# Kernel optimization log

Hardware: AMD Instinct MI355X
Metric: run time of the kernel (lower is better)

Reference implementation:

```python
import jax, jax.numpy as jnp
import numpy as np

N_NODES = 50000
N_EDGES = 800000
D = 128


def setup_inputs() -> dict:
    key = jax.random.key(0)
    ks = jax.random.split(key, 5)
    x = jax.random.normal(ks[0], (N_NODES, D), dtype=jnp.float32)
    edge_index = jax.random.randint(ks[1], (2, N_EDGES), 0, N_NODES, dtype=jnp.int64)
    # GCNConv linear weight + bias, and the two DGCN parameters
    Wc = jax.random.normal(ks[2], (D, D), dtype=jnp.float32) / np.sqrt(D)
    bc = jnp.zeros((D,), dtype=jnp.float32)
    W0 = jax.random.normal(ks[3], (D, D), dtype=jnp.float32)
    Wt = jax.random.normal(ks[4], (D, D), dtype=jnp.float32)
    return {"x": x, "edge_index": edge_index, "Wc": Wc, "bc": bc, "W0": W0, "Wt": Wt}


def gcn_conv(x, edge_index, Wc, bc):
    # PyG GCNConv: add self-loops, symmetric normalization D^-1/2 (A+I) D^-1/2,
    # applied to x @ Wc, plus bias.
    n = x.shape[0]
    loops = jnp.arange(n, dtype=edge_index.dtype)
    src = jnp.concatenate([edge_index[0], loops])  # [E+N]
    dst = jnp.concatenate([edge_index[1], loops])
    ones = jnp.ones(src.shape[0], dtype=x.dtype)
    deg = jax.ops.segment_sum(ones, dst, num_segments=n)  # in-degree incl. self-loop
    dinv = jnp.where(deg > 0, jax.lax.rsqrt(deg), 0.0)
    norm = dinv[src] * dinv[dst]  # [E+N]
    xw = x @ Wc  # [N, D]
    msgs = xw[src] * norm[:, None]  # gather + scale  [E+N, D]
    agg = jax.ops.segment_sum(msgs, dst, num_segments=n)  # scatter-add  [N, D]
    return agg + bc


def reference(x, edge_index, Wc, bc, W0, Wt):
    h_neigh = gcn_conv(x, edge_index, Wc, bc)
    h_self = x @ W0
    h_change = (h_neigh - x) @ Wt
    return h_neigh + h_self + h_change
```

## Files before the change

### kernel.cpp

```cpp
#include <hip/hip_runtime.h>

#define N_NODES 50000
#define N_EDGES 800000
#define D 128
#define NB 196
#define P1_BLOCKS 128
#define EPB ((N_EDGES + P1_BLOCKS - 1) / P1_BLOCKS)
#define CAP 64

typedef __attribute__((ext_vector_type(8))) short short8;
typedef __attribute__((ext_vector_type(4))) float f32x4;

__device__ __forceinline__ unsigned short f2bf(float f) {
    unsigned int u = __builtin_bit_cast(unsigned int, f);
    u += 0x7FFFu + ((u >> 16) & 1u);
    return (unsigned short)(u >> 16);
}
__device__ __forceinline__ float bf2f(unsigned short h) {
    unsigned int u = ((unsigned int)h) << 16;
    return __builtin_bit_cast(float, u);
}

__global__ __launch_bounds__(256) void k_bcnt(const int* __restrict__ dst,
                                              int* __restrict__ bcnt) {
    __shared__ int h[NB];
    const int t = threadIdx.x;
    for (int i = t; i < NB; i += 256) h[i] = 0;
    __syncthreads();
    const long e0 = (long)blockIdx.x * EPB;
    const long e1 = (e0 + EPB < N_EDGES) ? e0 + EPB : N_EDGES;
    for (long e = e0 + t; e < e1; e += 256) atomicAdd(&h[dst[e] >> 8], 1);
    __syncthreads();
    for (int i = t; i < NB; i += 256)
        if (h[i]) atomicAdd(&bcnt[i], h[i]);
}

__global__ __launch_bounds__(256) void k_bscan2(const int* __restrict__ bcnt,
                                                int* __restrict__ bucket_base,
                                                int* __restrict__ gcur) {
    __shared__ int s[256];
    const int t = threadIdx.x;
    const int v = (t < NB) ? bcnt[t] : 0;
    s[t] = v;
    __syncthreads();
    for (int off = 1; off < 256; off <<= 1) {
        int u = (t >= off) ? s[t - off] : 0;
        __syncthreads();
        s[t] += u;
        __syncthreads();
    }
    if (t < NB) {
        const int base = s[t] - v;
        bucket_base[t] = base;
        gcur[t] = base;
    }
}

__global__ __launch_bounds__(256) void k_part1(const int* __restrict__ src,
                                               const int* __restrict__ dst,
                                               int* __restrict__ gcur,
                                               unsigned int* __restrict__ pbuf) {
    __shared__ unsigned int stage[NB][CAP + 1];
    __shared__ int scnt[NB];
    const int t = threadIdx.x;
    for (int i = t; i < NB; i += 256) scnt[i] = 0;
    __syncthreads();

    const long e0 = (long)blockIdx.x * EPB;
    const long e1 = (e0 + EPB < N_EDGES) ? e0 + EPB : N_EDGES;
    for (long e = e0 + t; e < e1; e += 256) {
        const int s = src[e];
        const int d = dst[e];
        const int b = d >> 8;
        const unsigned int p = ((unsigned int)(d & 255) << 16) | (unsigned int)s;
        const int slot = atomicAdd(&scnt[b], 1);
        if (slot < CAP) {
            stage[b][slot] = p;
        } else {
            const int pos = atomicAdd(&gcur[b], 1);
            pbuf[pos] = p;
        }
    }
    __syncthreads();
    if (t < NB) {
        const int n = (scnt[t] < CAP) ? scnt[t] : CAP;
        if (n > 0) {
            const int pos = atomicAdd(&gcur[t], n);
            for (int i = 0; i < n; ++i) pbuf[pos + i] = stage[t][i];
        }
    }
}

__global__ __launch_bounds__(256) void k_part2(const unsigned int* __restrict__ pbuf,
                                               const int* __restrict__ bucket_base,
                                               const int* __restrict__ bcnt,
                                               int* __restrict__ row_start,
                                               int* __restrict__ cnt,
                                               float* __restrict__ dinv,
                                               int* __restrict__ esrc) {
    __shared__ int lcnt[256];
    __shared__ int lcur[256];
    __shared__ int stmp[256];
    const int b = blockIdx.x;
    const int t = threadIdx.x;
    const int base = bucket_base[b];
    const int n = bcnt[b];

    lcnt[t] = 0;
    __syncthreads();
    for (int i = t; i < n; i += 256) atomicAdd(&lcnt[pbuf[base + i] >> 16], 1);
    __syncthreads();

    const int c = lcnt[t];
    stmp[t] = c;
    __syncthreads();
    for (int off = 1; off < 256; off <<= 1) {
        int u = (t >= off) ? stmp[t - off] : 0;
        __syncthreads();
        stmp[t] += u;
        __syncthreads();
    }
    const int ls = base + stmp[t] - c;
    lcur[t] = ls;
    const int node = b * 256 + t;
    if (node < N_NODES) {
        row_start[node] = ls;
        cnt[node] = c;
        dinv[node] = rsqrtf((float)c + 1.0f);
    }
    __syncthreads();

    for (int i = t; i < n; i += 256) {
        const unsigned int p = pbuf[base + i];
        const int pos = atomicAdd(&lcur[p >> 16], 1);
        esrc[pos] = (int)(p & 0xFFFFu);
    }
}

__global__ __launch_bounds__(256) void k_wpack(const float* __restrict__ Wc,
                                               const float* __restrict__ W0,
                                               const float* __restrict__ Wt,
                                               const float* __restrict__ bc,
                                               unsigned short* __restrict__ Wp,
                                               float* __restrict__ bv) {
    __shared__ float sWt[D * D];
    const int t = threadIdx.x;
    for (int i = t * 4; i < D * D; i += 256 * 4)
        *(float4*)(sWt + i) = *(const float4*)(Wt + i);
    __syncthreads();

    if (blockIdx.x == 16) {
        if (t < D) {
            float acc = bc[t];
#pragma unroll 16
            for (int k = 0; k < D; ++k) acc += bc[k] * sWt[k * D + t];
            bv[t] = acc;
        }
        return;
    }
    const int id = blockIdx.x * 256 + t;
    const int lane = id & 63;
    const int tile = (id >> 6) & 7;
    const int step = id >> 9;
    const int n = tile * 16 + (lane & 15);
    const int kbase = step * 32 + (lane >> 4) * 8;
    unsigned short v[8];
#pragma unroll
    for (int j = 0; j < 8; ++j) {
        const int k = kbase + j;
        float f;
        if (k < D) {
            f = Wc[k * D + n];
#pragma unroll 16
            for (int m = 0; m < D; ++m) f += Wc[k * D + m] * sWt[m * D + n];
        } else {
            f = W0[(k - D) * D + n] - sWt[(k - D) * D + n];
        }
        v[j] = f2bf(f);
    }
    *(uint4*)(Wp + (long)id * 8) = *(uint4*)v;
}

__global__ __launch_bounds__(256) void k_xcast(const float* __restrict__ x,
                                               const float* __restrict__ dinv,
                                               unsigned short* __restrict__ xd,
                                               unsigned short* __restrict__ gx) {
    const int gid = blockIdx.x * 256 + threadIdx.x;
    const int node = gid >> 4;
    const int c = gid & 15;
    const float di = dinv[node];
    const float4 a = ((const float4*)x)[(long)node * 32 + c * 2];
    const float4 b = ((const float4*)x)[(long)node * 32 + c * 2 + 1];
    const float f[8] = {a.x, a.y, a.z, a.w, b.x, b.y, b.z, b.w};
    unsigned short vd[8], vb[8];
#pragma unroll
    for (int j = 0; j < 8; ++j) {
        vd[j] = f2bf(di * f[j]);
        vb[j] = f2bf(f[j]);
    }
    *(uint4*)(xd + (long)node * 128 + c * 8) = *(uint4*)vd;
    *(uint4*)(gx + (long)node * 256 + 128 + c * 8) = *(uint4*)vb;
}

__global__ __launch_bounds__(256) void k_gather(const unsigned short* __restrict__ xd,
                                                const int* __restrict__ row_start,
                                                const int* __restrict__ cnt,
                                                const int* __restrict__ esrc,
                                                const float* __restrict__ dinv,
                                                unsigned short* __restrict__ gx) {
    const int node = blockIdx.x * 4 + (threadIdx.x >> 6);
    const int lane = threadIdx.x & 63;
    const int c = lane & 15;
    const int s = lane >> 4;
    const int begin = row_start[node];
    const int end = begin + cnt[node];

    float acc[8] = {};
    int i = begin + s;
    for (; i + 4 < end; i += 8) {
        const int a0 = esrc[i];
        const int a1 = esrc[i + 4];
        const short8 v0 = *(const short8*)(xd + (long)a0 * 128 + c * 8);
        const short8 v1 = *(const short8*)(xd + (long)a1 * 128 + c * 8);
#pragma unroll
        for (int j = 0; j < 8; ++j)
            acc[j] += bf2f((unsigned short)v0[j]) + bf2f((unsigned short)v1[j]);
    }
    if (i < end) {
        const int a0 = esrc[i];
        const short8 v0 = *(const short8*)(xd + (long)a0 * 128 + c * 8);
#pragma unroll
        for (int j = 0; j < 8; ++j) acc[j] += bf2f((unsigned short)v0[j]);
    }

#pragma unroll
    for (int j = 0; j < 8; ++j) {
        acc[j] += __shfl_xor(acc[j], 16);
        acc[j] += __shfl_xor(acc[j], 32);
    }

    if (s == 0) {
        const float di = dinv[node];
        const short8 xs = *(const short8*)(xd + (long)node * 128 + c * 8);
        unsigned short o[8];
#pragma unroll
        for (int j = 0; j < 8; ++j)
            o[j] = f2bf(di * (acc[j] + bf2f((unsigned short)xs[j])));
        *(uint4*)(gx + (long)node * 256 + c * 8) = *(uint4*)o;
    }
}

__global__ __launch_bounds__(256) void k_mm(const unsigned short* __restrict__ gx,
                                            const unsigned short* __restrict__ Wp,
                                            const float* __restrict__ bv,
                                            float* __restrict__ out) {
    const int tid = threadIdx.x;
    const int wave = tid >> 6;
    const int lane = tid & 63;
    const int quad = lane >> 4;
    const int lr = lane & 15;
    const int row0 = blockIdx.x * 64 + wave * 16;

    int ar = row0 + lr;
    if (ar >= N_NODES) ar = N_NODES - 1;
    const unsigned short* aptr = gx + (long)ar * 256 + quad * 8;

    f32x4 acc[8] = {};

#pragma unroll
    for (int s = 0; s < 8; ++s) {
        const short8 a = *(const short8*)(aptr + s * 32);
#pragma unroll
        for (int t = 0; t < 8; ++t) {
            const short8 b = *(const short8*)(Wp + ((long)(s * 8 + t) * 64 + lane) * 8);
            acc[t] = __builtin_amdgcn_mfma_f32_16x16x32_bf16(a, b, acc[t], 0, 0, 0);
        }
    }

#pragma unroll
    for (int t = 0; t < 8; ++t) {
        const int col = t * 16 + lr;
        const float bvv = bv[col];
#pragma unroll
        for (int r = 0; r < 4; ++r) {
            const int row = row0 + quad * 4 + r;
            if (row < N_NODES) out[(long)row * D + col] = acc[t][r] + bvv;
        }
    }
}

extern "C" void kernel_launch(void* const* d_in, const int* in_sizes, int n_in,
                              void* d_out, int out_size, void* d_ws, size_t ws_size,
                              hipStream_t stream) {
    const float* x  = (const float*)d_in[0];
    const int*   ei = (const int*)d_in[1];
    const float* Wc = (const float*)d_in[2];
    const float* bc = (const float*)d_in[3];
    const float* W0 = (const float*)d_in[4];
    const float* Wt = (const float*)d_in[5];
    float* out = (float*)d_out;

    const int* src = ei;
    const int* dst = ei + N_EDGES;

    unsigned short* gx = (unsigned short*)d_ws;
    unsigned short* xd = gx + (size_t)N_NODES * 256;
    int*   cnt        = (int*)(xd + (size_t)N_NODES * 128);
    int*   row_start  = cnt + N_NODES;
    float* dinv       = (float*)(row_start + N_NODES);
    int*   esrc       = (int*)(dinv + N_NODES);
    unsigned int* pbuf = (unsigned int*)(esrc + N_EDGES);
    float* bv         = (float*)(pbuf + N_EDGES);
    unsigned short* Wp = (unsigned short*)(bv + D);
    int*   bcnt       = (int*)(Wp + 256 * D);
    int*   bucket_base = bcnt + NB;
    int*   gcur       = bucket_base + NB;

    hipMemsetAsync(bcnt, 0, NB * sizeof(int), stream);

    k_bcnt<<<P1_BLOCKS, 256, 0, stream>>>(dst, bcnt);
    k_bscan2<<<1, 256, 0, stream>>>(bcnt, bucket_base, gcur);
    k_part1<<<P1_BLOCKS, 256, 0, stream>>>(src, dst, gcur, pbuf);
    k_part2<<<NB, 256, 0, stream>>>(pbuf, bucket_base, bcnt, row_start, cnt, dinv, esrc);

    k_wpack<<<17, 256, 0, stream>>>(Wc, W0, Wt, bc, Wp, bv);

    k_xcast<<<(N_NODES * 16) / 256, 256, 0, stream>>>(x, dinv, xd, gx);

    k_gather<<<N_NODES / 4, 256, 0, stream>>>(xd, row_start, cnt, esrc, dinv, gx);

    k_mm<<<(N_NODES + 63) / 64, 256, 0, stream>>>(gx, Wp, bv, out);
}
```

Baseline: 197.8 us.

## Fuse neighbor gather into MFMA matmul, drop bucket-count pass, merge weight-pack and cast

```diff
diff --git a/kernel.cpp b/kernel.cpp
--- a/kernel.cpp
+++ b/kernel.cpp
@@ -4,9 +4,11 @@
 #define N_EDGES 800000
 #define D 128
 #define NB 196
+#define CAPB 8192
 #define P1_BLOCKS 128
 #define EPB ((N_EDGES + P1_BLOCKS - 1) / P1_BLOCKS)
 #define CAP 64
+#define GROWS 136
 
 typedef __attribute__((ext_vector_type(8))) short short8;
 typedef __attribute__((ext_vector_type(4))) float f32x4;
@@ -21,39 +23,9 @@
     return __builtin_bit_cast(float, u);
 }
 
-__global__ __launch_bounds__(256) void k_bcnt(const int* __restrict__ dst,
-                                              int* __restrict__ bcnt) {
-    __shared__ int h[NB];
+__global__ void k_init(int* __restrict__ gcur) {
     const int t = threadIdx.x;
-    for (int i = t; i < NB; i += 256) h[i] = 0;
-    __syncthreads();
-    const long e0 = (long)blockIdx.x * EPB;
-    const long e1 = (e0 + EPB < N_EDGES) ? e0 + EPB : N_EDGES;
-    for (long e = e0 + t; e < e1; e += 256) atomicAdd(&h[dst[e] >> 8], 1);
-    __syncthreads();
-    for (int i = t; i < NB; i += 256)
-        if (h[i]) atomicAdd(&bcnt[i], h[i]);
-}
-
-__global__ __launch_bounds__(256) void k_bscan2(const int* __restrict__ bcnt,
-                                                int* __restrict__ bucket_base,
-                                                int* __restrict__ gcur) {
-    __shared__ int s[256];
-    const int t = threadIdx.x;
-    const int v = (t < NB) ? bcnt[t] : 0;
-    s[t] = v;
-    __syncthreads();
-    for (int off = 1; off < 256; off <<= 1) {
-        int u = (t >= off) ? s[t - off] : 0;
-        __syncthreads();
-        s[t] += u;
-        __syncthreads();
-    }
-    if (t < NB) {
-        const int base = s[t] - v;
-        bucket_base[t] = base;
-        gcur[t] = base;
-    }
+    if (t < NB) gcur[t] = t * CAPB;
 }
 
 __global__ __launch_bounds__(256) void k_part1(const int* __restrict__ src,
@@ -92,8 +64,7 @@
 }
 
 __global__ __launch_bounds__(256) void k_part2(const unsigned int* __restrict__ pbuf,
-                                               const int* __restrict__ bucket_base,
-                                               const int* __restrict__ bcnt,
+                                               const int* __restrict__ gcur,
                                                int* __restrict__ row_start,
                                                int* __restrict__ cnt,
                                                float* __restrict__ dinv,
@@ -103,8 +74,8 @@
     __shared__ int stmp[256];
     const int b = blockIdx.x;
     const int t = threadIdx.x;
-    const int base = bucket_base[b];
-    const int n = bcnt[b];
+    const int base = b * CAPB;
+    const int n = gcur[b] - base;
 
     lcnt[t] = 0;
     __syncthreads();
@@ -137,55 +108,58 @@
     }
 }
 
-__global__ __launch_bounds__(256) void k_wpack(const float* __restrict__ Wc,
-                                               const float* __restrict__ W0,
-                                               const float* __restrict__ Wt,
-                                               const float* __restrict__ bc,
-                                               unsigned short* __restrict__ Wp,
-                                               float* __restrict__ bv) {
+__global__ __launch_bounds__(256) void k_wx(const float* __restrict__ Wc,
+                                            const float* __restrict__ W0,
+                                            const float* __restrict__ Wt,
+                                            const float* __restrict__ bc,
+                                            const float* __restrict__ x,
+                                            const float* __restrict__ dinv,
+                                            unsigned short* __restrict__ Wp,
+                                            float* __restrict__ bv,
+                                            unsigned short* __restrict__ xd,
+                                            unsigned short* __restrict__ xb) {
     __shared__ float sWt[D * D];
     const int t = threadIdx.x;
-    for (int i = t * 4; i < D * D; i += 256 * 4)
-        *(float4*)(sWt + i) = *(const float4*)(Wt + i);
-    __syncthreads();
-
-    if (blockIdx.x == 16) {
-        if (t < D) {
-            float acc = bc[t];
+
+    if (blockIdx.x < 17) {
+        for (int i = t * 4; i < D * D; i += 256 * 4)
+            *(float4*)(sWt + i) = *(const float4*)(Wt + i);
+        __syncthreads();
+
+        if (blockIdx.x == 16) {
+            if (t < D) {
+                float acc = bc[t];
 #pragma unroll 16
-            for (int k = 0; k < D; ++k) acc += bc[k] * sWt[k * D + t];
-            bv[t] = acc;
-        }
+                for (int k = 0; k < D; ++k) acc += bc[k] * sWt[k * D + t];
+                bv[t] = acc;
+            }
+            return;
+        }
+        const int id = blockIdx.x * 256 + t;
+        const int lane = id & 63;
+        const int tile = (id >> 6) & 7;
+        const int step = id >> 9;
+        const int n = tile * 16 + (lane & 15);
+        const int kbase = step * 32 + (lane >> 4) * 8;
+        unsigned short v[8];
+#pragma unroll
+        for (int j = 0; j < 8; ++j) {
+            const int k = kbase + j;
+            float f;
+            if (k < D) {
+                f = Wc[k * D + n];
+#pragma unroll 16
+                for (int m = 0; m < D; ++m) f += Wc[k * D + m] * sWt[m * D + n];
+            } else {
+                f = W0[(k - D) * D + n] - sWt[(k - D) * D + n];
+            }
+            v[j] = f2bf(f);
+        }
+        *(uint4*)(Wp + (long)id * 8) = *(uint4*)v;
         return;
     }
-    const int id = blockIdx.x * 256 + t;
-    const int lane = id & 63;
-    const int tile = (id >> 6) & 7;
-    const int step = id >> 9;
-    const int n = tile * 16 + (lane & 15);
-    const int kbase = step * 32 + (lane >> 4) * 8;
-    unsigned short v[8];
-#pragma unroll
-    for (int j = 0; j < 8; ++j) {
-        const int k = kbase + j;
-        float f;
-        if (k < D) {
-            f = Wc[k * D + n];
-#pragma unroll 16
-            for (int m = 0; m < D; ++m) f += Wc[k * D + m] * sWt[m * D + n];
-        } else {
-            f = W0[(k - D) * D + n] - sWt[(k - D) * D + n];
-        }
-        v[j] = f2bf(f);
-    }
-    *(uint4*)(Wp + (long)id * 8) = *(uint4*)v;
-}
-
-__global__ __launch_bounds__(256) void k_xcast(const float* __restrict__ x,
-                                               const float* __restrict__ dinv,
-                                               unsigned short* __restrict__ xd,
-                                               unsigned short* __restrict__ gx) {
-    const int gid = blockIdx.x * 256 + threadIdx.x;
+
+    const int gid = (blockIdx.x - 17) * 256 + t;
     const int node = gid >> 4;
     const int c = gid & 15;
     const float di = dinv[node];
@@ -199,81 +173,93 @@
         vb[j] = f2bf(f[j]);
     }
     *(uint4*)(xd + (long)node * 128 + c * 8) = *(uint4*)vd;
-    *(uint4*)(gx + (long)node * 256 + 128 + c * 8) = *(uint4*)vb;
-}
-
-__global__ __launch_bounds__(256) void k_gather(const unsigned short* __restrict__ xd,
-                                                const int* __restrict__ row_start,
-                                                const int* __restrict__ cnt,
-                                                const int* __restrict__ esrc,
-                                                const float* __restrict__ dinv,
-                                                unsigned short* __restrict__ gx) {
-    const int node = blockIdx.x * 4 + (threadIdx.x >> 6);
-    const int lane = threadIdx.x & 63;
-    const int c = lane & 15;
-    const int s = lane >> 4;
-    const int begin = row_start[node];
-    const int end = begin + cnt[node];
-
-    float acc[8] = {};
-    int i = begin + s;
-    for (; i + 4 < end; i += 8) {
-        const int a0 = esrc[i];
-        const int a1 = esrc[i + 4];
-        const short8 v0 = *(const short8*)(xd + (long)a0 * 128 + c * 8);
-        const short8 v1 = *(const short8*)(xd + (long)a1 * 128 + c * 8);
-#pragma unroll
-        for (int j = 0; j < 8; ++j)
-            acc[j] += bf2f((unsigned short)v0[j]) + bf2f((unsigned short)v1[j]);
-    }
-    if (i < end) {
-        const int a0 = esrc[i];
-        const short8 v0 = *(const short8*)(xd + (long)a0 * 128 + c * 8);
-#pragma unroll
-        for (int j = 0; j < 8; ++j) acc[j] += bf2f((unsigned short)v0[j]);
-    }
-
-#pragma unroll
-    for (int j = 0; j < 8; ++j) {
-        acc[j] += __shfl_xor(acc[j], 16);
-        acc[j] += __shfl_xor(acc[j], 32);
-    }
-
-    if (s == 0) {
-        const float di = dinv[node];
-        const short8 xs = *(const short8*)(xd + (long)node * 128 + c * 8);
-        unsigned short o[8];
-#pragma unroll
-        for (int j = 0; j < 8; ++j)
-            o[j] = f2bf(di * (acc[j] + bf2f((unsigned short)xs[j])));
-        *(uint4*)(gx + (long)node * 256 + c * 8) = *(uint4*)o;
-    }
-}
-
-__global__ __launch_bounds__(256) void k_mm(const unsigned short* __restrict__ gx,
-                                            const unsigned short* __restrict__ Wp,
-                                            const float* __restrict__ bv,
-                                            float* __restrict__ out) {
+    *(uint4*)(xb + (long)node * 128 + c * 8) = *(uint4*)vb;
+}
+
+__global__ __launch_bounds__(256) void k_gmm(const unsigned short* __restrict__ xd,
+                                             const unsigned short* __restrict__ xb,
+                                             const int* __restrict__ row_start,
+                                             const int* __restrict__ cnt,
+                                             const int* __restrict__ esrc,
+                                             const float* __restrict__ dinv,
+                                             const unsigned short* __restrict__ Wp,
+                                             const float* __restrict__ bv,
+                                             float* __restrict__ out) {
+    __shared__ unsigned short gl[4][16][GROWS];
     const int tid = threadIdx.x;
     const int wave = tid >> 6;
     const int lane = tid & 63;
-    const int quad = lane >> 4;
     const int lr = lane & 15;
+    const int sl = lane >> 4;
     const int row0 = blockIdx.x * 64 + wave * 16;
+
+    const int myrow = row0 + lr;
+    int vbegin = 0, vcnt = 0;
+    float vdinv = 0.f;
+    if (lr < 16 && myrow < N_NODES) {
+        vbegin = row_start[myrow];
+        vcnt = cnt[myrow];
+        vdinv = dinv[myrow];
+    }
+
+    for (int r = 0; r < 16; ++r) {
+        const int node = row0 + r;
+        const int begin = __shfl(vbegin, r);
+        const int end = begin + __shfl(vcnt, r);
+        float acc[8] = {};
+        int i = begin + sl;
+        for (; i + 4 < end; i += 8) {
+            const int a0 = esrc[i];
+            const int a1 = esrc[i + 4];
+            const short8 v0 = *(const short8*)(xd + (long)a0 * 128 + lr * 8);
+            const short8 v1 = *(const short8*)(xd + (long)a1 * 128 + lr * 8);
+#pragma unroll
+            for (int j = 0; j < 8; ++j)
+                acc[j] += bf2f((unsigned short)v0[j]) + bf2f((unsigned short)v1[j]);
+        }
+        if (i < end) {
+            const int a0 = esrc[i];
+            const short8 v0 = *(const short8*)(xd + (long)a0 * 128 + lr * 8);
+#pragma unroll
+            for (int j = 0; j < 8; ++j) acc[j] += bf2f((unsigned short)v0[j]);
+        }
+#pragma unroll
+        for (int j = 0; j < 8; ++j) {
+            acc[j] += __shfl_xor(acc[j], 16);
+            acc[j] += __shfl_xor(acc[j], 32);
+        }
+        if (sl == 0) {
+            const float di = __shfl(vdinv, r);
+            const int nn = (node < N_NODES) ? node : 0;
+            const short8 xs = *(const short8*)(xd + (long)nn * 128 + lr * 8);
+            unsigned short o[8];
+#pragma unroll
+            for (int j = 0; j < 8; ++j)
+                o[j] = f2bf(di * (acc[j] + bf2f((unsigned short)xs[j])));
+            *(uint4*)(&gl[wave][r][lr * 8]) = *(uint4*)o;
+        }
+    }
 
     int ar = row0 + lr;
     if (ar >= N_NODES) ar = N_NODES - 1;
-    const unsigned short* aptr = gx + (long)ar * 256 + quad * 8;
-
-    f32x4 acc[8] = {};
-
-#pragma unroll
-    for (int s = 0; s < 8; ++s) {
-        const short8 a = *(const short8*)(aptr + s * 32);
+
+    f32x4 accm[8] = {};
+#pragma unroll
+    for (int s = 0; s < 4; ++s) {
+        const short8 a = *(const short8*)(&gl[wave][lr][s * 32 + sl * 8]);
 #pragma unroll
         for (int t = 0; t < 8; ++t) {
             const short8 b = *(const short8*)(Wp + ((long)(s * 8 + t) * 64 + lane) * 8);
-            acc[t] = __builtin_amdgcn_mfma_f32_16x16x32_bf16(a, b, acc[t], 0, 0, 0);
+            accm[t] = __builtin_amdgcn_mfma_f32_16x16x32_bf16(a, b, accm[t], 0, 0, 0);
+        }
+    }
+#pragma unroll
+    for (int s = 4; s < 8; ++s) {
+        const short8 a = *(const short8*)(xb + (long)ar * 128 + (s - 4) * 32 + sl * 8);
+#pragma unroll
+        for (int t = 0; t < 8; ++t) {
+            const short8 b = *(const short8*)(Wp + ((long)(s * 8 + t) * 64 + lane) * 8);
+            accm[t] = __builtin_amdgcn_mfma_f32_16x16x32_bf16(a, b, accm[t], 0, 0, 0);
         }
     }
 
@@ -283,8 +269,8 @@
         const float bvv = bv[col];
 #pragma unroll
         for (int r = 0; r < 4; ++r) {
-            const int row = row0 + quad * 4 + r;
-            if (row < N_NODES) out[(long)row * D + col] = acc[t][r] + bvv;
+            const int row = row0 + sl * 4 + r;
+            if (row < N_NODES) out[(long)row * D + col] = accm[t][r] + bvv;
         }
     }
 }
@@ -303,31 +289,22 @@
     const int* src = ei;
     const int* dst = ei + N_EDGES;
 
-    unsigned short* gx = (unsigned short*)d_ws;
-    unsigned short* xd = gx + (size_t)N_NODES * 256;
-    int*   cnt        = (int*)(xd + (size_t)N_NODES * 128);
+    unsigned short* xd = (unsigned short*)d_ws;
+    unsigned short* xb = xd + (size_t)N_NODES * 128;
+    int*   cnt        = (int*)(xb + (size_t)N_NODES * 128);
     int*   row_start  = cnt + N_NODES;
     float* dinv       = (float*)(row_start + N_NODES);
     int*   esrc       = (int*)(dinv + N_NODES);
-    unsigned int* pbuf = (unsigned int*)(esrc + N_EDGES);
-    float* bv         = (float*)(pbuf + N_EDGES);
+    unsigned int* pbuf = (unsigned int*)(esrc + (size_t)NB * CAPB);
+    float* bv         = (float*)(pbuf + (size_t)NB * CAPB);
     unsigned short* Wp = (unsigned short*)(bv + D);
-    int*   bcnt       = (int*)(Wp + 256 * D);
-    int*   bucket_base = bcnt + NB;
-    int*   gcur       = bucket_base + NB;
-
-    hipMemsetAsync(bcnt, 0, NB * sizeof(int), stream);
-
-    k_bcnt<<<P1_BLOCKS, 256, 0, stream>>>(dst, bcnt);
-    k_bscan2<<<1, 256, 0, stream>>>(bcnt, bucket_base, gcur);
+    int*   gcur       = (int*)(Wp + 256 * D);
+
+    k_init<<<1, 256, 0, stream>>>(gcur);
     k_part1<<<P1_BLOCKS, 256, 0, stream>>>(src, dst, gcur, pbuf);
-    k_part2<<<NB, 256, 0, stream>>>(pbuf, bucket_base, bcnt, row_start, cnt, dinv, esrc);
-
-    k_wpack<<<17, 256, 0, stream>>>(Wc, W0, Wt, bc, Wp, bv);
-
-    k_xcast<<<(N_NODES * 16) / 256, 256, 0, stream>>>(x, dinv, xd, gx);
-
-    k_gather<<<N_NODES / 4, 256, 0, stream>>>(xd, row_start, cnt, esrc, dinv, gx);
-
-    k_mm<<<(N_NODES + 63) / 64, 256, 0, stream>>>(gx, Wp, bv, out);
-}
+    k_part2<<<NB, 256, 0, stream>>>(pbuf, gcur, row_start, cnt, dinv, esrc);
+    k_wx<<<17 + (N_NODES * 16) / 256, 256, 0, stream>>>(Wc, W0, Wt, bc, x, dinv,
+                                                        Wp, bv, xd, xb);
+    k_gmm<<<(N_NODES + 63) / 64, 256, 0, stream>>>(xd, xb, row_start, cnt, esrc,
+                                                   dinv, Wp, bv, out);
+}
```

New measurement: 188.5 us. -4.7%, faster.

## Replace bucket count/scan with fixed-capacity buckets, fuse weight pack and cast, unroll gather

Applied to the files above, without the earlier changes.

```diff
diff --git a/kernel.cpp b/kernel.cpp
--- a/kernel.cpp
+++ b/kernel.cpp
@@ -4,7 +4,8 @@
 #define N_EDGES 800000
 #define D 128
 #define NB 196
-#define P1_BLOCKS 128
+#define CAPB 8192
+#define P1_BLOCKS 256
 #define EPB ((N_EDGES + P1_BLOCKS - 1) / P1_BLOCKS)
 #define CAP 64
 
@@ -21,39 +22,9 @@
     return __builtin_bit_cast(float, u);
 }
 
-__global__ __launch_bounds__(256) void k_bcnt(const int* __restrict__ dst,
-                                              int* __restrict__ bcnt) {
-    __shared__ int h[NB];
+__global__ void k_init(int* __restrict__ gcur) {
     const int t = threadIdx.x;
-    for (int i = t; i < NB; i += 256) h[i] = 0;
-    __syncthreads();
-    const long e0 = (long)blockIdx.x * EPB;
-    const long e1 = (e0 + EPB < N_EDGES) ? e0 + EPB : N_EDGES;
-    for (long e = e0 + t; e < e1; e += 256) atomicAdd(&h[dst[e] >> 8], 1);
-    __syncthreads();
-    for (int i = t; i < NB; i += 256)
-        if (h[i]) atomicAdd(&bcnt[i], h[i]);
-}
-
-__global__ __launch_bounds__(256) void k_bscan2(const int* __restrict__ bcnt,
-                                                int* __restrict__ bucket_base,
-                                                int* __restrict__ gcur) {
-    __shared__ int s[256];
-    const int t = threadIdx.x;
-    const int v = (t < NB) ? bcnt[t] : 0;
-    s[t] = v;
-    __syncthreads();
-    for (int off = 1; off < 256; off <<= 1) {
-        int u = (t >= off) ? s[t - off] : 0;
-        __syncthreads();
-        s[t] += u;
-        __syncthreads();
-    }
-    if (t < NB) {
-        const int base = s[t] - v;
-        bucket_base[t] = base;
-        gcur[t] = base;
-    }
+    if (t < NB) gcur[t] = t * CAPB;
 }
 
 __global__ __launch_bounds__(256) void k_part1(const int* __restrict__ src,
@@ -92,8 +63,7 @@
 }
 
 __global__ __launch_bounds__(256) void k_part2(const unsigned int* __restrict__ pbuf,
-                                               const int* __restrict__ bucket_base,
-                                               const int* __restrict__ bcnt,
+                                               const int* __restrict__ gcur,
                                                int* __restrict__ row_start,
                                                int* __restrict__ cnt,
                                                float* __restrict__ dinv,
@@ -103,8 +73,8 @@
     __shared__ int stmp[256];
     const int b = blockIdx.x;
     const int t = threadIdx.x;
-    const int base = bucket_base[b];
-    const int n = bcnt[b];
+    const int base = b * CAPB;
+    const int n = gcur[b] - base;
 
     lcnt[t] = 0;
     __syncthreads();
@@ -137,55 +107,58 @@
     }
 }
 
-__global__ __launch_bounds__(256) void k_wpack(const float* __restrict__ Wc,
-                                               const float* __restrict__ W0,
-                                               const float* __restrict__ Wt,
-                                               const float* __restrict__ bc,
-                                               unsigned short* __restrict__ Wp,
-                                               float* __restrict__ bv) {
+__global__ __launch_bounds__(256) void k_wx(const float* __restrict__ Wc,
+                                            const float* __restrict__ W0,
+                                            const float* __restrict__ Wt,
+                                            const float* __restrict__ bc,
+                                            const float* __restrict__ x,
+                                            const float* __restrict__ dinv,
+                                            unsigned short* __restrict__ Wp,
+                                            float* __restrict__ bv,
+                                            unsigned short* __restrict__ xd,
+                                            unsigned short* __restrict__ gx) {
     __shared__ float sWt[D * D];
     const int t = threadIdx.x;
-    for (int i = t * 4; i < D * D; i += 256 * 4)
-        *(float4*)(sWt + i) = *(const float4*)(Wt + i);
-    __syncthreads();
-
-    if (blockIdx.x == 16) {
-        if (t < D) {
-            float acc = bc[t];
+
+    if (blockIdx.x < 17) {
+        for (int i = t * 4; i < D * D; i += 256 * 4)
+            *(float4*)(sWt + i) = *(const float4*)(Wt + i);
+        __syncthreads();
+
+        if (blockIdx.x == 16) {
+            if (t < D) {
+                float acc = bc[t];
 #pragma unroll 16
-            for (int k = 0; k < D; ++k) acc += bc[k] * sWt[k * D + t];
-            bv[t] = acc;
-        }
+                for (int k = 0; k < D; ++k) acc += bc[k] * sWt[k * D + t];
+                bv[t] = acc;
+            }
+            return;
+        }
+        const int id = blockIdx.x * 256 + t;
+        const int lane = id & 63;
+        const int tile = (id >> 6) & 7;
+        const int step = id >> 9;
+        const int n = tile * 16 + (lane & 15);
+        const int kbase = step * 32 + (lane >> 4) * 8;
+        unsigned short v[8];
+#pragma unroll
+        for (int j = 0; j < 8; ++j) {
+            const int k = kbase + j;
+            float f;
+            if (k < D) {
+                f = Wc[k * D + n];
+#pragma unroll 16
+                for (int m = 0; m < D; ++m) f += Wc[k * D + m] * sWt[m * D + n];
+            } else {
+                f = W0[(k - D) * D + n] - sWt[(k - D) * D + n];
+            }
+            v[j] = f2bf(f);
+        }
+        *(uint4*)(Wp + (long)id * 8) = *(uint4*)v;
         return;
     }
-    const int id = blockIdx.x * 256 + t;
-    const int lane = id & 63;
-    const int tile = (id >> 6) & 7;
-    const int step = id >> 9;
-    const int n = tile * 16 + (lane & 15);
-    const int kbase = step * 32 + (lane >> 4) * 8;
-    unsigned short v[8];
-#pragma unroll
-    for (int j = 0; j < 8; ++j) {
-        const int k = kbase + j;
-        float f;
-        if (k < D) {
-            f = Wc[k * D + n];
-#pragma unroll 16
-            for (int m = 0; m < D; ++m) f += Wc[k * D + m] * sWt[m * D + n];
-        } else {
-            f = W0[(k - D) * D + n] - sWt[(k - D) * D + n];
-        }
-        v[j] = f2bf(f);
-    }
-    *(uint4*)(Wp + (long)id * 8) = *(uint4*)v;
-}
-
-__global__ __launch_bounds__(256) void k_xcast(const float* __restrict__ x,
-                                               const float* __restrict__ dinv,
-                                               unsigned short* __restrict__ xd,
-                                               unsigned short* __restrict__ gx) {
-    const int gid = blockIdx.x * 256 + threadIdx.x;
+
+    const int gid = (blockIdx.x - 17) * 256 + t;
     const int node = gid >> 4;
     const int c = gid & 15;
     const float di = dinv[node];
@@ -217,16 +190,21 @@
 
     float acc[8] = {};
     int i = begin + s;
-    for (; i + 4 < end; i += 8) {
+    for (; i + 12 < end; i += 16) {
         const int a0 = esrc[i];
         const int a1 = esrc[i + 4];
+        const int a2 = esrc[i + 8];
+        const int a3 = esrc[i + 12];
         const short8 v0 = *(const short8*)(xd + (long)a0 * 128 + c * 8);
         const short8 v1 = *(const short8*)(xd + (long)a1 * 128 + c * 8);
+        const short8 v2 = *(const short8*)(xd + (long)a2 * 128 + c * 8);
+        const short8 v3 = *(const short8*)(xd + (long)a3 * 128 + c * 8);
 #pragma unroll
         for (int j = 0; j < 8; ++j)
-            acc[j] += bf2f((unsigned short)v0[j]) + bf2f((unsigned short)v1[j]);
-    }
-    if (i < end) {
+            acc[j] += (bf2f((unsigned short)v0[j]) + bf2f((unsigned short)v1[j])) +
+                      (bf2f((unsigned short)v2[j]) + bf2f((unsigned short)v3[j]));
+    }
+    for (; i < end; i += 4) {
         const int a0 = esrc[i];
         const short8 v0 = *(const short8*)(xd + (long)a0 * 128 + c * 8);
 #pragma unroll
@@ -303,31 +281,22 @@
     const int* src = ei;
     const int* dst = ei + N_EDGES;
 
-    unsigned short* gx = (unsigned short*)d_ws;
-    unsigned short* xd = gx + (size_t)N_NODES * 256;
-    int*   cnt        = (int*)(xd + (size_t)N_NODES * 128);
+    unsigned short* xd = (unsigned short*)d_ws;
+    unsigned short* gx = xd + (size_t)N_NODES * 128;
+    int*   cnt        = (int*)(gx + (size_t)N_NODES * 256);
     int*   row_start  = cnt + N_NODES;
     float* dinv       = (float*)(row_start + N_NODES);
     int*   esrc       = (int*)(dinv + N_NODES);
-    unsigned int* pbuf = (unsigned int*)(esrc + N_EDGES);
-    float* bv         = (float*)(pbuf + N_EDGES);
+    unsigned int* pbuf = (unsigned int*)(esrc + (size_t)NB * CAPB);
+    float* bv         = (float*)(pbuf + (size_t)NB * CAPB);
     unsigned short* Wp = (unsigned short*)(bv + D);
-    int*   bcnt       = (int*)(Wp + 256 * D);
-    int*   bucket_base = bcnt + NB;
-    int*   gcur       = bucket_base + NB;
-
-    hipMemsetAsync(bcnt, 0, NB * sizeof(int), stream);
-
-    k_bcnt<<<P1_BLOCKS, 256, 0, stream>>>(dst, bcnt);
-    k_bscan2<<<1, 256, 0, stream>>>(bcnt, bucket_base, gcur);
+    int*   gcur       = (int*)(Wp + 256 * D);
+
+    k_init<<<1, 256, 0, stream>>>(gcur);
     k_part1<<<P1_BLOCKS, 256, 0, stream>>>(src, dst, gcur, pbuf);
-    k_part2<<<NB, 256, 0, stream>>>(pbuf, bucket_base, bcnt, row_start, cnt, dinv, esrc);
-
-    k_wpack<<<17, 256, 0, stream>>>(Wc, W0, Wt, bc, Wp, bv);
-
-    k_xcast<<<(N_NODES * 16) / 256, 256, 0, stream>>>(x, dinv, xd, gx);
-
+    k_part2<<<NB, 256, 0, stream>>>(pbuf, gcur, row_start, cnt, dinv, esrc);
+    k_wx<<<17 + (N_NODES * 16) / 256, 256, 0, stream>>>(Wc, W0, Wt, bc, x, dinv,
+                                                        Wp, bv, xd, gx);
     k_gather<<<N_NODES / 4, 256, 0, stream>>>(xd, row_start, cnt, esrc, dinv, gx);
-
     k_mm<<<(N_NODES + 63) / 64, 256, 0, stream>>>(gx, Wp, bv, out);
 }
```

New measurement: 178.4 us. 9.8% less time.
